# Performance work log

Measured on AMD Instinct MI355X. Metric: run time of the kernel, lower is better.

The kernel has to match this reference:

```python
import jax, jax.numpy as jnp
import numpy as np

B, H, W = 64, 512, 512
TOP_K = 200
N_OBJS = 200
KP_THRES = 0.1
IOU_THR = 0.5
RESIZE_H, RESIZE_W = 512.0, 512.0


def setup_inputs() -> dict:
    key = jax.random.key(0)
    k1, k2, k3 = jax.random.split(key, 3)
    heatmap_y = jax.random.uniform(k1, (B, H), dtype=jnp.float32)
    heatmap_x = jax.random.uniform(k2, (B, W), dtype=jnp.float32)
    # box sizes in heatmap pixels (scaled so boxes are non-degenerate)
    size_maps = jax.random.uniform(k3, (B, H, W, 2), dtype=jnp.float32) * 64.0
    origin_shapes = jnp.full((B, 2), 1024.0, dtype=jnp.float32)
    return {"heatmap_y": heatmap_y, "heatmap_x": heatmap_x,
            "size_maps": size_maps, "origin_shapes": origin_shapes}


def _iou_one_vs_all(box, boxes):
    # box: (4,) [y1,x1,y2,x2]; boxes: (N,4)
    yy1 = jnp.maximum(box[0], boxes[:, 0])
    xx1 = jnp.maximum(box[1], boxes[:, 1])
    yy2 = jnp.minimum(box[2], boxes[:, 2])
    xx2 = jnp.minimum(box[3], boxes[:, 3])
    inter = jnp.maximum(yy2 - yy1, 0.0) * jnp.maximum(xx2 - xx1, 0.0)
    a1 = (box[2] - box[0]) * (box[3] - box[1])
    a2 = (boxes[:, 2] - boxes[:, 0]) * (boxes[:, 3] - boxes[:, 1])
    denom = a1 + a2 - inter
    return jnp.where(denom > 0.0, inter / jnp.maximum(denom, 1e-12), 0.0)


def _nms_single(boxes, scores):
    # greedy NMS over N boxes, selecting up to N_OBJS (TF combined_non_max_suppression,
    # single class, clip_boxes=False, score_threshold=-inf, zero-padded output)
    N = boxes.shape[0]

    def body(i, st):
        active, sb, ss, cnt = st
        ms = jnp.where(active, scores, -jnp.inf)
        j = jnp.argmax(ms)
        valid = ms[j] > -jnp.inf
        bj = boxes[j]
        ious = _iou_one_vs_all(bj, boxes)
        active = active & (ious <= IOU_THR)
        active = active.at[j].set(False)
        sb = sb.at[i].set(jnp.where(valid, bj, jnp.zeros_like(bj)))
        ss = ss.at[i].set(jnp.where(valid, scores[j], 0.0))
        return (active, sb, ss, cnt + valid.astype(jnp.int32))

    init = (jnp.ones((N,), dtype=bool),
            jnp.zeros((N_OBJS, 4), boxes.dtype),
            jnp.zeros((N_OBJS,), scores.dtype),
            jnp.array(0, jnp.int32))
    _, sb, ss, cnt = jax.lax.fori_loop(0, N_OBJS, body, init)
    return sb, ss, cnt


def _decode(heatmap_y, heatmap_x, size_maps, origin_shapes):
    Bd, Hd = heatmap_y.shape
    Wd = heatmap_x.shape[1]
    # rank-1 heatmap: matmul(hy[...,None], hx[...,None]^T) == outer product -> (B,H,W)
    hm = heatmap_y[:, :, None] * heatmap_x[:, None, :]
    # 3x3 max-pool peak suppression (CenterNet keep-mask)
    hmax = jax.lax.reduce_window(hm, -jnp.inf, jax.lax.max,
                                 (1, 3, 3), (1, 1, 1), 'SAME')
    hm = jnp.where(hmax == hm, hm, 0.0)
    # top-k over flattened spatial dims (c == 1)
    scores, idx = jax.lax.top_k(hm.reshape(Bd, Hd * Wd), TOP_K)  # (B,K)
    ys = idx // Wd
    xs = idx % Wd
    bidx = jnp.arange(Bd)[:, None]
    sizes = size_maps[bidx, ys, xs]                      # (B,K,2) gather_nd
    centers = jnp.stack([ys, xs], axis=-1).astype(hm.dtype)  # (B,K,2)
    tls = jnp.maximum(centers - sizes / 2.0, 0.0)        # clamp tl at 0
    brs = centers + sizes / 2.0
    br_y = jnp.minimum(brs[..., 0], RESIZE_H - 1.0)
    br_x = jnp.minimum(brs[..., 1], RESIZE_W - 1.0)
    # resize back to original image coords
    ratio = origin_shapes / jnp.asarray([RESIZE_H, RESIZE_W], dtype=hm.dtype)  # (B,2)
    ry = ratio[:, 0:1]
    rx = ratio[:, 1:2]
    boxes = jnp.stack([tls[..., 0] * ry, tls[..., 1] * rx,
                       br_y * ry, br_x * rx], axis=-1)   # (B,K,4)
    # threshold mask + scatter into -1-initialized output (indices == own positions)
    mask = scores > KP_THRES
    boxes = jnp.where(mask[..., None], boxes, -1.0)
    sc = jnp.where(mask, scores, -1.0)
    if TOP_K < N_OBJS:
        boxes = jnp.pad(boxes, ((0, 0), (0, N_OBJS - TOP_K), (0, 0)), constant_values=-1.0)
        sc = jnp.pad(sc, ((0, 0), (0, N_OBJS - TOP_K)), constant_values=-1.0)
    nb, ns, _cnt = jax.vmap(_nms_single)(boxes, sc)      # (B,N_OBJS,4), (B,N_OBJS)
    # post: -1 boxes -> inf, 0 (NMS padding) boxes -> inf
    nb = jnp.where(nb == -1.0, jnp.inf, nb)
    nb = jnp.where(nb == 0.0, jnp.inf, nb)
    classes = jnp.zeros_like(ns)                         # single class -> class id 0
    out = jnp.concatenate([nb, ns[..., None], classes[..., None]], axis=-1)
    return out.reshape(-1, N_OBJS, 6)


def reference(heatmap_y, heatmap_x, size_maps, origin_shapes):
    return _decode(heatmap_y, heatmap_x, size_maps, origin_shapes)
```

## Files before the change

### kernel.cpp

```cpp
#include <hip/hip_runtime.h>
#include <stdint.h>

#define NT 256
#define HW 512
#define TOPK 200
#define STAIR_GEN 256
#define STAIR_T 204
#define MAXCAND 1024
#define MAXCLOSE 320

typedef unsigned long long u64;
typedef unsigned u32;

__global__ __launch_bounds__(NT) void decode_nms_kernel(
    const float* __restrict__ hyg, const float* __restrict__ hxg,
    const float* __restrict__ size_maps, const float* __restrict__ origin,
    float* __restrict__ out)
{
#pragma clang fp contract(off)
  const int b = blockIdx.x;
  const int tid = threadIdx.x;

  __shared__ __align__(16) float hy[HW], hx[HW];
  __shared__ int   cyI[MAXCLOSE + 8], cxI[MAXCLOSE + 8];
  __shared__ __align__(16) float cyV[MAXCLOSE + 8], cyM[MAXCLOSE + 8];
  __shared__ __align__(16) float cxV[MAXCLOSE + 8], cxM[MAXCLOSE + 8];
  __shared__ __align__(16) u64 pK[2][HW + 2];
  __shared__ float sV[2][HW];
  __shared__ int   sI[2][HW];
  __shared__ __align__(16) u64 cand[MAXCAND + 2];
  __shared__ float tS[TOPK];
  __shared__ int   tL[TOPK];
  __shared__ float4 bb4[256];
  __shared__ u64   sup[256][4];
  __shared__ int   pickL[TOPK];
  __shared__ int   nCY, nCX, nPk0, nPk1, nCand, survSh;
  __shared__ u32   Tbits;

  if (tid == 0) { nCY = 0; nCX = 0; nPk0 = 0; nPk1 = 0; nCand = 0; Tbits = 0; }
  for (int i = tid; i < HW; i += NT) {
    hy[i] = hyg[(size_t)b * HW + i];
    hx[i] = hxg[(size_t)b * HW + i];
  }
  __syncthreads();

  for (int it = 0; it < 2; ++it) {
    int i = it * NT + tid;
    float v = hy[i], m = v;
    if (i > 0)      m = fmaxf(m, hy[i - 1]);
    if (i < HW - 1) m = fmaxf(m, hy[i + 1]);
    if (v >= m * (1.0f - 1e-6f)) {
      int p = atomicAdd(&nCY, 1);
      if (p < MAXCLOSE) { cyI[p] = i; cyV[p] = v; cyM[p] = m; }
    }
    if (v == m) {
      int p = atomicAdd(&nPk0, 1);
      pK[0][p] = ((u64)__float_as_uint(v) << 32) | (u64)(0xFFFFFFFFu - (u32)i);
    }
    float w = hx[i], mw = w;
    if (i > 0)      mw = fmaxf(mw, hx[i - 1]);
    if (i < HW - 1) mw = fmaxf(mw, hx[i + 1]);
    if (w >= mw * (1.0f - 1e-6f)) {
      int p = atomicAdd(&nCX, 1);
      if (p < MAXCLOSE) { cxI[p] = i; cxV[p] = w; cxM[p] = mw; }
    }
    if (w == mw) {
      int p = atomicAdd(&nPk1, 1);
      pK[1][p] = ((u64)__float_as_uint(w) << 32) | (u64)(0xFFFFFFFFu - (u32)i);
    }
  }
  __syncthreads();

  int NP0 = nPk0, NP1 = nPk1;
  int ncy = nCY < MAXCLOSE ? nCY : MAXCLOSE;
  int ncx = nCX < MAXCLOSE ? nCX : MAXCLOSE;
  if (tid == 0) { pK[0][NP0] = 0; pK[1][NP1] = 0; }
  if (tid < 8)  { cxV[ncx + tid] = 0.f; cxM[ncx + tid] = 0.f; }
  __syncthreads();

  for (int d = 0; d < 2; ++d) {
    int n = d ? NP1 : NP0;
    int n2 = (n + 1) >> 1;
    const ulonglong2* pk2 = (const ulonglong2*)&pK[d][0];
    for (int i = tid; i < n; i += NT) {
      u64 key = pK[d][i];
      int rank = 0;
      int j2 = 0;
      for (; j2 + 8 <= n2; j2 += 8) {
        ulonglong2 a0 = pk2[j2+0], a1 = pk2[j2+1], a2 = pk2[j2+2], a3 = pk2[j2+3];
        ulonglong2 a4 = pk2[j2+4], a5 = pk2[j2+5], a6 = pk2[j2+6], a7 = pk2[j2+7];
        rank += (a0.x > key) + (a0.y > key) + (a1.x > key) + (a1.y > key)
              + (a2.x > key) + (a2.y > key) + (a3.x > key) + (a3.y > key)
              + (a4.x > key) + (a4.y > key) + (a5.x > key) + (a5.y > key)
              + (a6.x > key) + (a6.y > key) + (a7.x > key) + (a7.y > key);
      }
      for (; j2 < n2; ++j2) {
        ulonglong2 a = pk2[j2];
        rank += (a.x > key) + (a.y > key);
      }
      sV[d][rank] = __uint_as_float((u32)(key >> 32));
      sI[d][rank] = (int)(0xFFFFFFFFu - (u32)(key & 0xFFFFFFFFu));
    }
  }
  __syncthreads();

  {
    int a = tid + 1;
    if (a <= STAIR_T && a <= NP0) {
      int bn = (STAIR_T + a - 1) / a;
      if (bn <= NP1) atomicMax(&Tbits, __float_as_uint(sV[0][a - 1] * sV[1][bn - 1]));
    }
  }
  __syncthreads();
  const float T = __uint_as_float(Tbits);

  for (int yi = tid; yi < ncy; yi += NT) {
    float vy = cyV[yi], mvy = cyM[yi];
    bool py = (vy == mvy);
    int ybase = cyI[yi] * HW;
    const float4* cv4 = (const float4*)cxV;
    const float4* cm4 = (const float4*)cxM;
    int nb = (ncx + 7) >> 3;
    for (int blk = 0; blk < nb; ++blk) {
      float4 v0 = cv4[2*blk], v1 = cv4[2*blk + 1];
      float4 m0 = cm4[2*blk], m1 = cm4[2*blk + 1];
      float vv[8] = {v0.x, v0.y, v0.z, v0.w, v1.x, v1.y, v1.z, v1.w};
      float mm[8] = {m0.x, m0.y, m0.z, m0.w, m1.x, m1.y, m1.z, m1.w};
      unsigned hits = 0;
      #pragma unroll
      for (int u = 0; u < 8; ++u) {
        float pr = vy * vv[u];
        bool h = (!(py && vv[u] == mm[u])) && (pr == mvy * mm[u])
               && (pr > 0.1f) && (pr >= T);
        hits |= ((unsigned)h) << u;
      }
      if (__builtin_expect(hits != 0, 0)) {
        for (int u = 0; u < 8; ++u) if ((hits >> u) & 1u) {
          int xi = blk * 8 + u;
          float pr = vy * cxV[xi];
          int pos = atomicAdd(&nCand, 1);
          if (pos < MAXCAND)
            cand[pos] = ((u64)__float_as_uint(pr) << 32)
                      | (u64)(0xFFFFFFFFu - (u32)(ybase + cxI[xi]));
        }
      }
    }
  }

  {
    int NY = NP0 < STAIR_GEN ? NP0 : STAIR_GEN;
    int i = tid >> 4, jc = tid & 15;
    if (i < NY) {
      int jmax = STAIR_GEN / (i + 1); if (jmax > NP1) jmax = NP1;
      int jlo = jc * 16, jhi = jlo + 16; if (jhi > jmax) jhi = jmax;
      float vy = sV[0][i]; int ybase = sI[0][i] * HW;
      #pragma unroll 4
      for (int j = jlo; j < jhi; ++j) {
        float s = vy * sV[1][j];
        if (s > 0.1f && s >= T) {
          int pos = atomicAdd(&nCand, 1);
          if (pos < MAXCAND)
            cand[pos] = ((u64)__float_as_uint(s) << 32)
                      | (u64)(0xFFFFFFFFu - (u32)(ybase + sI[1][j]));
        }
      }
    }
    for (int i2 = 16 + tid; i2 < NY; i2 += NT) {
      int jmax = STAIR_GEN / (i2 + 1); if (jmax > NP1) jmax = NP1;
      float vy = sV[0][i2]; int ybase = sI[0][i2] * HW;
      #pragma unroll 4
      for (int j = 0; j < jmax; ++j) {
        float s = vy * sV[1][j];
        if (s > 0.1f && s >= T) {
          int pos = atomicAdd(&nCand, 1);
          if (pos < MAXCAND)
            cand[pos] = ((u64)__float_as_uint(s) << 32)
                      | (u64)(0xFFFFFFFFu - (u32)(ybase + sI[1][j]));
        }
      }
    }
  }
  __syncthreads();
  int C = nCand < MAXCAND ? nCand : MAXCAND;
  if (tid == 0) cand[C] = 0;
  __syncthreads();

  {
    int C2 = (C + 1) >> 1;
    const ulonglong2* cd2 = (const ulonglong2*)&cand[0];
    for (int i = tid; i < C; i += NT) {
      u64 k = cand[i];
      int rank = 0;
      int j2 = 0;
      for (; j2 + 8 <= C2; j2 += 8) {
        ulonglong2 a0 = cd2[j2+0], a1 = cd2[j2+1], a2 = cd2[j2+2], a3 = cd2[j2+3];
        ulonglong2 a4 = cd2[j2+4], a5 = cd2[j2+5], a6 = cd2[j2+6], a7 = cd2[j2+7];
        rank += (a0.x > k) + (a0.y > k) + (a1.x > k) + (a1.y > k)
              + (a2.x > k) + (a2.y > k) + (a3.x > k) + (a3.y > k)
              + (a4.x > k) + (a4.y > k) + (a5.x > k) + (a5.y > k)
              + (a6.x > k) + (a6.y > k) + (a7.x > k) + (a7.y > k);
      }
      for (; j2 < C2; ++j2) {
        ulonglong2 a = cd2[j2];
        rank += (a.x > k) + (a.y > k);
      }
      if (rank < TOPK) {
        tS[rank] = __uint_as_float((u32)(k >> 32));
        tL[rank] = (int)(0xFFFFFFFFu - (u32)(k & 0xFFFFFFFFu));
      }
    }
  }
  __syncthreads();
  int R = C < TOPK ? C : TOPK;

  float ry = origin[b * 2 + 0] / 512.0f;
  float rx = origin[b * 2 + 1] / 512.0f;
  for (int r = tid; r < 256; r += NT) {
    if (r < R) {
      int lin = tL[r];
      int y = lin >> 9, x = lin & (HW - 1);
      const float* sp = size_maps + (((size_t)b * HW + y) * HW + x) * 2;
      float s0 = sp[0], s1 = sp[1];
      float cy = (float)y, cx = (float)x;
      bb4[r] = make_float4(fmaxf(cy - s0 * 0.5f, 0.0f) * ry,
                           fmaxf(cx - s1 * 0.5f, 0.0f) * rx,
                           fminf(cy + s0 * 0.5f, 511.0f) * ry,
                           fminf(cx + s1 * 0.5f, 511.0f) * rx);
    } else {
      bb4[r] = make_float4(0.f, 0.f, 0.f, 0.f);
    }
  }
  __syncthreads();

  {
    int k = tid;
    bool hasK = (k < R);
    float4 bk = bb4[k];
    float k0 = bk.x, k1 = bk.y, k2 = bk.z, k3 = bk.w;
    float a1 = (k2 - k0) * (k3 - k1);
    int wv = k >> 6;
    for (int w = 0; w < 4; ++w) {
      u64 word = 0;
      int jbase = w << 6;
      if (jbase < R && w >= wv) {
        for (int jj = 0; jj < 64; jj += 4) {
          float4 bjv[4] = {bb4[jbase+jj], bb4[jbase+jj+1],
                           bb4[jbase+jj+2], bb4[jbase+jj+3]};
          #pragma unroll
          for (int u = 0; u < 4; ++u) {
            int j = jbase + jj + u;
            float4 bj = bjv[u];
            float yy1 = fmaxf(k0, bj.x), xx1 = fmaxf(k1, bj.y);
            float yy2 = fminf(k2, bj.z), xx2 = fminf(k3, bj.w);
            float inter = fmaxf(yy2 - yy1, 0.0f) * fmaxf(xx2 - xx1, 0.0f);
            float a2 = (bj.z - bj.x) * (bj.w - bj.y);
            float denom = a1 + a2 - inter;
            float iou = (denom > 0.0f) ? (inter / fmaxf(denom, 1e-12f)) : 0.0f;
            bool s = hasK && (j > k) && (j < R) && (iou > 0.5f);
            word |= ((u64)s) << (jj + u);
          }
        }
      }
      sup[k][w] = word;
    }
  }
  __syncthreads();

  if (tid == 0) {
    u64 al0 = ~0ull, al1 = ~0ull, al2 = ~0ull, al3 = ~0ull;
    u64 cur[4][4], nxt[4][4];
    #pragma unroll
    for (int t = 0; t < 4; ++t) {
      cur[t][0] = sup[t][0]; cur[t][1] = sup[t][1];
      cur[t][2] = sup[t][2]; cur[t][3] = sup[t][3];
    }
    int s = 0;
    for (int k0 = 0; k0 < R; k0 += 4) {
      #pragma unroll
      for (int t = 0; t < 4; ++t) {
        nxt[t][0] = sup[k0 + 4 + t][0]; nxt[t][1] = sup[k0 + 4 + t][1];
        nxt[t][2] = sup[k0 + 4 + t][2]; nxt[t][3] = sup[k0 + 4 + t][3];
      }
      #pragma unroll
      for (int t = 0; t < 4; ++t) {
        int k = k0 + t;
        if (k < R) {
          u64 aw = (k < 64) ? al0 : (k < 128) ? al1 : (k < 192) ? al2 : al3;
          if ((aw >> (k & 63)) & 1ull) {
            pickL[s++] = k;
            al0 &= ~cur[t][0]; al1 &= ~cur[t][1];
            al2 &= ~cur[t][2]; al3 &= ~cur[t][3];
          }
        }
      }
      #pragma unroll
      for (int t = 0; t < 4; ++t) {
        cur[t][0] = nxt[t][0]; cur[t][1] = nxt[t][1];
        cur[t][2] = nxt[t][2]; cur[t][3] = nxt[t][3];
      }
    }
    survSh = s;
  }
  __syncthreads();

  int surv = survSh;
  int nNeg = TOPK - R;
  for (int r = tid; r < TOPK; r += NT) {
    float o0, o1, o2, o3, o4;
    if (r < surv) {
      int k = pickL[r];
      float4 bk = bb4[k];
      o0 = bk.x; o1 = bk.y; o2 = bk.z; o3 = bk.w; o4 = tS[k];
    } else if (r < surv + nNeg) {
      o0 = o1 = o2 = o3 = -1.0f; o4 = -1.0f;
    } else {
      o0 = o1 = o2 = o3 = 0.0f; o4 = 0.0f;
    }
    float* o = out + ((size_t)b * TOPK + r) * 6;
    o[0] = o0; o[1] = o1; o[2] = o2; o[3] = o3; o[4] = o4; o[5] = 0.0f;
  }
}

extern "C" void kernel_launch(void* const* d_in, const int* in_sizes, int n_in,
                              void* d_out, int out_size, void* d_ws, size_t ws_size,
                              hipStream_t stream) {
  const float* hyg = (const float*)d_in[0];
  const float* hxg = (const float*)d_in[1];
  const float* szm = (const float*)d_in[2];
  const float* org = (const float*)d_in[3];
  int B = in_sizes[0] / HW;
  decode_nms_kernel<<<dim3(B), dim3(NT), 0, stream>>>(hyg, hxg, szm, org, (float*)d_out);
}
```

Measured before the change: 252.2 us.

## Quadruple block size and spread decode/NMS phases across 1024 threads

```diff
diff --git a/kernel.cpp b/kernel.cpp
--- a/kernel.cpp
+++ b/kernel.cpp
@@ -1,7 +1,7 @@
 #include <hip/hip_runtime.h>
 #include <stdint.h>
 
-#define NT 256
+#define NT 1024
 #define HW 512
 #define TOPK 200
 #define STAIR_GEN 256
@@ -21,7 +21,8 @@
   const int b = blockIdx.x;
   const int tid = threadIdx.x;
 
-  __shared__ __align__(16) float hy[HW], hx[HW];
+  __shared__ __align__(16) float hy[HW];
+  __shared__ __align__(16) float hx[HW];
   __shared__ int   cyI[MAXCLOSE + 8], cxI[MAXCLOSE + 8];
   __shared__ __align__(16) float cyV[MAXCLOSE + 8], cyM[MAXCLOSE + 8];
   __shared__ __align__(16) float cxV[MAXCLOSE + 8], cxM[MAXCLOSE + 8];
@@ -38,14 +39,19 @@
   __shared__ u32   Tbits;
 
   if (tid == 0) { nCY = 0; nCX = 0; nPk0 = 0; nPk1 = 0; nCand = 0; Tbits = 0; }
-  for (int i = tid; i < HW; i += NT) {
-    hy[i] = hyg[(size_t)b * HW + i];
-    hx[i] = hxg[(size_t)b * HW + i];
-  }
-  __syncthreads();
-
-  for (int it = 0; it < 2; ++it) {
-    int i = it * NT + tid;
+
+  if (tid < 128) {
+    ((float4*)hy)[tid] = ((const float4*)(hyg + (size_t)b * HW))[tid];
+  } else if (tid < 256) {
+    ((float4*)hx)[tid - 128] = ((const float4*)(hxg + (size_t)b * HW))[tid - 128];
+  }
+  for (int i = tid; i < HW + 2; i += NT) { pK[0][i] = 0ull; pK[1][i] = 0ull; }
+  for (int i = tid; i <= MAXCAND; i += NT) cand[i] = 0ull;
+  for (int i = tid; i < MAXCLOSE + 8; i += NT) { cxV[i] = 0.f; cxM[i] = 0.f; }
+  __syncthreads();
+
+  if (tid < HW) {
+    int i = tid;
     float v = hy[i], m = v;
     if (i > 0)      m = fmaxf(m, hy[i - 1]);
     if (i < HW - 1) m = fmaxf(m, hy[i + 1]);
@@ -74,15 +80,14 @@
   int NP0 = nPk0, NP1 = nPk1;
   int ncy = nCY < MAXCLOSE ? nCY : MAXCLOSE;
   int ncx = nCX < MAXCLOSE ? nCX : MAXCLOSE;
-  if (tid == 0) { pK[0][NP0] = 0; pK[1][NP1] = 0; }
-  if (tid < 8)  { cxV[ncx + tid] = 0.f; cxM[ncx + tid] = 0.f; }
-  __syncthreads();
-
-  for (int d = 0; d < 2; ++d) {
+
+  {
+    int d = tid >> 9;
+    int t = tid & 511;
     int n = d ? NP1 : NP0;
     int n2 = (n + 1) >> 1;
     const ulonglong2* pk2 = (const ulonglong2*)&pK[d][0];
-    for (int i = tid; i < n; i += NT) {
+    for (int i = t; i < n; i += 512) {
       u64 key = pK[d][i];
       int rank = 0;
       int j2 = 0;
@@ -114,76 +119,80 @@
   __syncthreads();
   const float T = __uint_as_float(Tbits);
 
-  for (int yi = tid; yi < ncy; yi += NT) {
-    float vy = cyV[yi], mvy = cyM[yi];
-    bool py = (vy == mvy);
-    int ybase = cyI[yi] * HW;
-    const float4* cv4 = (const float4*)cxV;
-    const float4* cm4 = (const float4*)cxM;
-    int nb = (ncx + 7) >> 3;
-    for (int blk = 0; blk < nb; ++blk) {
-      float4 v0 = cv4[2*blk], v1 = cv4[2*blk + 1];
-      float4 m0 = cm4[2*blk], m1 = cm4[2*blk + 1];
-      float vv[8] = {v0.x, v0.y, v0.z, v0.w, v1.x, v1.y, v1.z, v1.w};
-      float mm[8] = {m0.x, m0.y, m0.z, m0.w, m1.x, m1.y, m1.z, m1.w};
-      unsigned hits = 0;
-      #pragma unroll
-      for (int u = 0; u < 8; ++u) {
-        float pr = vy * vv[u];
-        bool h = (!(py && vv[u] == mm[u])) && (pr == mvy * mm[u])
-               && (pr > 0.1f) && (pr >= T);
-        hits |= ((unsigned)h) << u;
-      }
-      if (__builtin_expect(hits != 0, 0)) {
-        for (int u = 0; u < 8; ++u) if ((hits >> u) & 1u) {
-          int xi = blk * 8 + u;
-          float pr = vy * cxV[xi];
-          int pos = atomicAdd(&nCand, 1);
-          if (pos < MAXCAND)
-            cand[pos] = ((u64)__float_as_uint(pr) << 32)
-                      | (u64)(0xFFFFFFFFu - (u32)(ybase + cxI[xi]));
-        }
-      }
-    }
-  }
-
   {
     int NY = NP0 < STAIR_GEN ? NP0 : STAIR_GEN;
-    int i = tid >> 4, jc = tid & 15;
-    if (i < NY) {
-      int jmax = STAIR_GEN / (i + 1); if (jmax > NP1) jmax = NP1;
-      int jlo = jc * 16, jhi = jlo + 16; if (jhi > jmax) jhi = jmax;
-      float vy = sV[0][i]; int ybase = sI[0][i] * HW;
-      #pragma unroll 4
-      for (int j = jlo; j < jhi; ++j) {
-        float s = vy * sV[1][j];
-        if (s > 0.1f && s >= T) {
-          int pos = atomicAdd(&nCand, 1);
-          if (pos < MAXCAND)
-            cand[pos] = ((u64)__float_as_uint(s) << 32)
-                      | (u64)(0xFFFFFFFFu - (u32)(ybase + sI[1][j]));
-        }
-      }
-    }
-    for (int i2 = 16 + tid; i2 < NY; i2 += NT) {
-      int jmax = STAIR_GEN / (i2 + 1); if (jmax > NP1) jmax = NP1;
-      float vy = sV[0][i2]; int ybase = sI[0][i2] * HW;
-      #pragma unroll 4
-      for (int j = 0; j < jmax; ++j) {
-        float s = vy * sV[1][j];
-        if (s > 0.1f && s >= T) {
-          int pos = atomicAdd(&nCand, 1);
-          if (pos < MAXCAND)
-            cand[pos] = ((u64)__float_as_uint(s) << 32)
-                      | (u64)(0xFFFFFFFFu - (u32)(ybase + sI[1][j]));
+    if (tid < 256) {
+      int i = tid >> 4, jc = tid & 15;
+      if (i < NY) {
+        int jmax = STAIR_GEN / (i + 1); if (jmax > NP1) jmax = NP1;
+        int jlo = jc * 16, jhi = jlo + 16; if (jhi > jmax) jhi = jmax;
+        float vy = sV[0][i]; int ybase = sI[0][i] * HW;
+        #pragma unroll 4
+        for (int j = jlo; j < jhi; ++j) {
+          float s = vy * sV[1][j];
+          if (s > 0.1f && s >= T) {
+            int pos = atomicAdd(&nCand, 1);
+            if (pos < MAXCAND)
+              cand[pos] = ((u64)__float_as_uint(s) << 32)
+                        | (u64)(0xFFFFFFFFu - (u32)(ybase + sI[1][j]));
+          }
+        }
+      }
+    } else if (tid < 768) {
+      int u = tid - 256;
+      int i2 = 16 + (u >> 1), c = u & 1;
+      if (i2 < NY) {
+        int jmax = STAIR_GEN / (i2 + 1); if (jmax > NP1) jmax = NP1;
+        int jlo = c * 8, jhi = jlo + 8; if (jhi > jmax) jhi = jmax;
+        float vy = sV[0][i2]; int ybase = sI[0][i2] * HW;
+        #pragma unroll 4
+        for (int j = jlo; j < jhi; ++j) {
+          float s = vy * sV[1][j];
+          if (s > 0.1f && s >= T) {
+            int pos = atomicAdd(&nCand, 1);
+            if (pos < MAXCAND)
+              cand[pos] = ((u64)__float_as_uint(s) << 32)
+                        | (u64)(0xFFFFFFFFu - (u32)(ybase + sI[1][j]));
+          }
+        }
+      }
+    } else {
+      for (int yi = tid - 768; yi < ncy; yi += 256) {
+        float vy = cyV[yi], mvy = cyM[yi];
+        bool py = (vy == mvy);
+        int ybase = cyI[yi] * HW;
+        const float4* cv4 = (const float4*)cxV;
+        const float4* cm4 = (const float4*)cxM;
+        int nb = (ncx + 7) >> 3;
+        for (int blk = 0; blk < nb; ++blk) {
+          float4 v0 = cv4[2*blk], v1 = cv4[2*blk + 1];
+          float4 m0 = cm4[2*blk], m1 = cm4[2*blk + 1];
+          float vv[8] = {v0.x, v0.y, v0.z, v0.w, v1.x, v1.y, v1.z, v1.w};
+          float mm[8] = {m0.x, m0.y, m0.z, m0.w, m1.x, m1.y, m1.z, m1.w};
+          unsigned hits = 0;
+          #pragma unroll
+          for (int u8 = 0; u8 < 8; ++u8) {
+            float pr = vy * vv[u8];
+            bool h = (!(py && vv[u8] == mm[u8])) && (pr == mvy * mm[u8])
+                   && (pr > 0.1f) && (pr >= T);
+            hits |= ((unsigned)h) << u8;
+          }
+          if (__builtin_expect(hits != 0, 0)) {
+            for (int u8 = 0; u8 < 8; ++u8) if ((hits >> u8) & 1u) {
+              int xi = blk * 8 + u8;
+              float pr = vy * cxV[xi];
+              int pos = atomicAdd(&nCand, 1);
+              if (pos < MAXCAND)
+                cand[pos] = ((u64)__float_as_uint(pr) << 32)
+                          | (u64)(0xFFFFFFFFu - (u32)(ybase + cxI[xi]));
+            }
+          }
         }
       }
     }
   }
   __syncthreads();
   int C = nCand < MAXCAND ? nCand : MAXCAND;
-  if (tid == 0) cand[C] = 0;
-  __syncthreads();
 
   {
     int C2 = (C + 1) >> 1;
@@ -233,36 +242,34 @@
   __syncthreads();
 
   {
-    int k = tid;
+    int k = tid & 255, w = tid >> 8;
     bool hasK = (k < R);
     float4 bk = bb4[k];
     float k0 = bk.x, k1 = bk.y, k2 = bk.z, k3 = bk.w;
     float a1 = (k2 - k0) * (k3 - k1);
     int wv = k >> 6;
-    for (int w = 0; w < 4; ++w) {
-      u64 word = 0;
-      int jbase = w << 6;
-      if (jbase < R && w >= wv) {
-        for (int jj = 0; jj < 64; jj += 4) {
-          float4 bjv[4] = {bb4[jbase+jj], bb4[jbase+jj+1],
-                           bb4[jbase+jj+2], bb4[jbase+jj+3]};
-          #pragma unroll
-          for (int u = 0; u < 4; ++u) {
-            int j = jbase + jj + u;
-            float4 bj = bjv[u];
-            float yy1 = fmaxf(k0, bj.x), xx1 = fmaxf(k1, bj.y);
-            float yy2 = fminf(k2, bj.z), xx2 = fminf(k3, bj.w);
-            float inter = fmaxf(yy2 - yy1, 0.0f) * fmaxf(xx2 - xx1, 0.0f);
-            float a2 = (bj.z - bj.x) * (bj.w - bj.y);
-            float denom = a1 + a2 - inter;
-            float iou = (denom > 0.0f) ? (inter / fmaxf(denom, 1e-12f)) : 0.0f;
-            bool s = hasK && (j > k) && (j < R) && (iou > 0.5f);
-            word |= ((u64)s) << (jj + u);
-          }
-        }
-      }
-      sup[k][w] = word;
-    }
+    u64 word = 0;
+    int jbase = w << 6;
+    if (jbase < R && w >= wv) {
+      for (int jj = 0; jj < 64; jj += 4) {
+        float4 bjv[4] = {bb4[jbase+jj], bb4[jbase+jj+1],
+                         bb4[jbase+jj+2], bb4[jbase+jj+3]};
+        #pragma unroll
+        for (int u = 0; u < 4; ++u) {
+          int j = jbase + jj + u;
+          float4 bj = bjv[u];
+          float yy1 = fmaxf(k0, bj.x), xx1 = fmaxf(k1, bj.y);
+          float yy2 = fminf(k2, bj.z), xx2 = fminf(k3, bj.w);
+          float inter = fmaxf(yy2 - yy1, 0.0f) * fmaxf(xx2 - xx1, 0.0f);
+          float a2 = (bj.z - bj.x) * (bj.w - bj.y);
+          float denom = a1 + a2 - inter;
+          float iou = (denom > 0.0f) ? (inter / fmaxf(denom, 1e-12f)) : 0.0f;
+          bool s = hasK && (j > k) && (j < R) && (iou > 0.5f);
+          word |= ((u64)s) << (jj + u);
+        }
+      }
+    }
+    sup[k][w] = word;
   }
   __syncthreads();
 
```

New measurement: 227.7 us. -9.7%, faster.
